# Performance work log

Measured on AMD Instinct MI355X. Metric: run time of the kernel, lower is better.

The kernel has to match this reference:

```python
import jax, jax.numpy as jnp
import numpy as np

B, S, C, L, E, A, H = 4, 4, 4, 512, 64, 32, 8


def _xavier(k, shape, fan_in, fan_out):
    lim = float(np.sqrt(6.0 / (fan_in + fan_out)))
    return jax.random.uniform(k, shape, jnp.float32, -lim, lim)


def setup_inputs() -> dict:
    key = jax.random.key(0)
    ks = jax.random.split(key, 14)
    inp = {
        "query_sequences": jax.random.normal(ks[0], (B, S, L, E), jnp.float32),
        "key_sequences": jax.random.normal(ks[1], (B, S, L, E), jnp.float32),
        "value_sequences": jax.random.normal(ks[2], (B, S, L, E), jnp.float32),
        "query_constants": jax.random.normal(ks[3], (B, C, 1, E), jnp.float32),
        "key_constants": jax.random.normal(ks[4], (B, C, 1, E), jnp.float32),
        "value_constants": jax.random.normal(ks[5], (B, C, 1, E), jnp.float32),
        "qw_seq": _xavier(ks[6], (S, H, E, A), E, A),
        "kw_seq": _xavier(ks[7], (S, H, E, A), E, A),
        "vw_seq": _xavier(ks[8], (S, H, E, A), E, A),
        "qw_con": _xavier(ks[9], (C, H, E, A), E, A),
        "kw_con": _xavier(ks[10], (C, H, E, A), E, A),
        "vw_con": _xavier(ks[11], (C, H, E, A), E, A),
        "head_w_seq": _xavier(ks[12], (S, H * A, E), H * A, E),
        "head_w_con": _xavier(ks[13], (C, H * A, E), H * A, E),
        "mask": 1,
    }
    return inp


def reference(query_sequences, key_sequences, value_sequences,
              query_constants, key_constants, value_constants,
              qw_seq, kw_seq, vw_seq, qw_con, kw_con, vw_con,
              head_w_seq, head_w_con, mask):
    # Per-sequence / per-constant, per-head QKV projections
    q_s = jnp.einsum('bsle,shea->bshla', query_sequences, qw_seq)      # [B,S,H,L,A]
    q_c = jnp.einsum('bcle,chea->bchla', query_constants, qw_con)      # [B,C,H,1,A]
    k_s = jnp.einsum('bsle,shea->bhsla', key_sequences, kw_seq).reshape(B, H, S * L, A)
    k_c = jnp.einsum('bcle,chea->bhcla', key_constants, kw_con).reshape(B, H, C, A)
    v_s = jnp.einsum('bsle,shea->bhsla', value_sequences, vw_seq).reshape(B, H, S * L, A)
    v_c = jnp.einsum('bcle,chea->bhcla', value_constants, vw_con).reshape(B, H, C, A)
    k_all = jnp.concatenate([k_s, k_c], axis=2)                        # [B,H,K,A], K=S*L+C
    v_all = jnp.concatenate([v_s, v_c], axis=2)

    scale = 1.0 / jnp.sqrt(jnp.asarray(A, jnp.float32))
    scores_s = jnp.einsum('bshla,bhka->bshlk', q_s, k_all) * scale     # [B,S,H,L,K]
    if mask:
        # block-causal: within each of the S key blocks mask future timesteps;
        # constant columns (time index -1) are always visible.
        kt = jnp.concatenate([jnp.tile(jnp.arange(L), S), jnp.full((C,), -1)])
        m = kt[None, :] > jnp.arange(L)[:, None]                       # [L,K]
        scores_s = jnp.where(m, -jnp.inf, scores_s)
    p_s = jax.nn.softmax(scores_s, axis=-1)
    out_s = jnp.einsum('bshlk,bhka->bslha', p_s, v_all).reshape(B, S, L, H * A)
    seq_out = jnp.einsum('bslf,sfe->bsle', out_s, head_w_seq)          # [B,S,L,E]

    scores_c = jnp.einsum('bchla,bhka->bchlk', q_c, k_all) * scale     # [B,C,H,1,K]
    p_c = jax.nn.softmax(scores_c, axis=-1)
    out_c = jnp.einsum('bchlk,bhka->bclha', p_c, v_all).reshape(B, C, 1, H * A)
    con_out = jnp.einsum('bclf,cfe->bcle', out_c, head_w_con)          # [B,C,1,E]
    return (seq_out, con_out)
```

## Files before the change

kernel.cpp:

```cpp
#include <hip/hip_runtime.h>
#include <hip/hip_bf16.h>

#define B_ 4
#define S_ 4
#define C_ 4
#define L_ 512
#define E_ 64
#define A_ 32
#define H_ 8
#define HA_ 256
#define KREAL 2052
#define KP 2112
#define NKT 33
#define SCALE 0.17677669529663687f
#define SCALE2 0.25503486321392056f
#define NEGINF (-__builtin_inff())

using bf16  = __bf16;
using bf16x8 = __attribute__((ext_vector_type(8))) __bf16;
using f32x4  = __attribute__((ext_vector_type(4))) float;

#define OFF_QS    0ull
#define OFF_KALL  4194304ull
#define OFF_VT    8519680ull
#define OFF_OUTS  12845056ull
#define OFF_OUTC  17039360ull

__device__ __forceinline__ bool detect_f32_fast(const unsigned int* __restrict__ x0)
{
  unsigned v = x0[threadIdx.x & 63];
  int e = (int)((v >> 7) & 0xFF);
  bool weird = (e == 0xFF || e < 0x60 || e > 0x9F);
  unsigned long long m = __ballot(weird);
  return __builtin_popcountll(m) > 16;
}

__device__ __forceinline__ bf16x8 ld8(const void* p, size_t idx, bool isf32) {
  if (isf32) {
    const float* f = (const float*)p + idx;
    float4 lo = *(const float4*)f;
    float4 hi = *(const float4*)(f + 4);
    bf16x8 v;
    v[0] = (bf16)lo.x; v[1] = (bf16)lo.y; v[2] = (bf16)lo.z; v[3] = (bf16)lo.w;
    v[4] = (bf16)hi.x; v[5] = (bf16)hi.y; v[6] = (bf16)hi.z; v[7] = (bf16)hi.w;
    return v;
  }
  return *(const bf16x8*)((const bf16*)p + idx);
}
__device__ __forceinline__ float ldf(const void* p, size_t idx, bool isf32) {
  return isf32 ? ((const float*)p)[idx] : (float)((const bf16*)p)[idx];
}

__global__ __launch_bounds__(256) void proj_kernel(
    const void* __restrict__ xq, const void* __restrict__ xk, const void* __restrict__ xv,
    const void* __restrict__ kc_in, const void* __restrict__ vc_in,
    const void* __restrict__ wq, const void* __restrict__ wk, const void* __restrict__ wv,
    const void* __restrict__ wkc, const void* __restrict__ wvc,
    bf16* __restrict__ qs, bf16* __restrict__ kall, bf16* __restrict__ vt)
{
  bool isf32 = detect_f32_fast((const unsigned int*)xq);
  int bid = blockIdx.x;
  int tid = threadIdx.x;
  if (bid < 1024) {
    int h = bid & 7, lc8 = (bid >> 3) & 7, s = (bid >> 6) & 3, b = (bid >> 8) & 3;
    __shared__ bf16 wt[3 * 32 * 72];
    __shared__ bf16 v_lds[32 * 72];
    {
      size_t hb = (size_t)(s * H_ + h) * E_ * A_;
      int e = tid >> 2, ac = tid & 3;
      bf16x8 vq = ld8(wq, hb + e * 32 + ac * 8, isf32);
      bf16x8 vk = ld8(wk, hb + e * 32 + ac * 8, isf32);
      bf16x8 vv = ld8(wv, hb + e * 32 + ac * 8, isf32);
#pragma unroll
      for (int j = 0; j < 8; ++j) {
        int a = ac * 8 + j;
        wt[0 * 2304 + a * 72 + e] = vq[j];
        wt[1 * 2304 + a * 72 + e] = vk[j];
        wt[2 * 2304 + a * 72 + e] = vv[j];
      }
    }
    __syncthreads();
    int lane = tid & 63, wave = tid >> 6;
    int quad = lane >> 4, r = lane & 15;
    const size_t xbase = (size_t)(b * S_ + s) * L_ * E_;
    const size_t qsb   = (size_t)((b * S_ + s) * H_ + h) * L_ * A_;
    const size_t kab   = (size_t)(b * H_ + h) * KP * A_;
    const size_t vtb   = (size_t)(b * H_ + h) * A_ * KP;
    int lloc0 = wave * 16;
    int row0 = lc8 * 64 + lloc0;
    size_t rowoff = xbase + (size_t)(row0 + r) * E_ + quad * 8;
    bf16x8 aq0 = ld8(xq, rowoff, isf32);
    bf16x8 aq1 = ld8(xq, rowoff + 32, isf32);
    bf16x8 ak0 = ld8(xk, rowoff, isf32);
    bf16x8 ak1 = ld8(xk, rowoff + 32, isf32);
    bf16x8 av0 = ld8(xv, rowoff, isf32);
    bf16x8 av1 = ld8(xv, rowoff + 32, isf32);
#pragma unroll
    for (int nt = 0; nt < 2; ++nt) {
      bf16x8 bq0 = *(const bf16x8*)&wt[(nt * 16 + r) * 72 + 0 + quad * 8];
      bf16x8 bq1 = *(const bf16x8*)&wt[(nt * 16 + r) * 72 + 32 + quad * 8];
      bf16x8 bk0 = *(const bf16x8*)&wt[2304 + (nt * 16 + r) * 72 + 0 + quad * 8];
      bf16x8 bk1 = *(const bf16x8*)&wt[2304 + (nt * 16 + r) * 72 + 32 + quad * 8];
      bf16x8 bv0 = *(const bf16x8*)&wt[4608 + (nt * 16 + r) * 72 + 0 + quad * 8];
      bf16x8 bv1 = *(const bf16x8*)&wt[4608 + (nt * 16 + r) * 72 + 32 + quad * 8];
      f32x4 accq = {0.f,0.f,0.f,0.f}, acck = {0.f,0.f,0.f,0.f}, accv = {0.f,0.f,0.f,0.f};
      accq = __builtin_amdgcn_mfma_f32_16x16x32_bf16(aq0, bq0, accq, 0,0,0);
      accq = __builtin_amdgcn_mfma_f32_16x16x32_bf16(aq1, bq1, accq, 0,0,0);
      acck = __builtin_amdgcn_mfma_f32_16x16x32_bf16(ak0, bk0, acck, 0,0,0);
      acck = __builtin_amdgcn_mfma_f32_16x16x32_bf16(ak1, bk1, acck, 0,0,0);
      accv = __builtin_amdgcn_mfma_f32_16x16x32_bf16(av0, bv0, accv, 0,0,0);
      accv = __builtin_amdgcn_mfma_f32_16x16x32_bf16(av1, bv1, accv, 0,0,0);
#pragma unroll
      for (int reg = 0; reg < 4; ++reg) {
        int l = row0 + quad * 4 + reg;
        int a = nt * 16 + r;
        qs[qsb + (size_t)l * A_ + a]              = (bf16)(accq[reg] * SCALE2);
        kall[kab + (size_t)(s * L_ + l) * A_ + a] = (bf16)acck[reg];
        v_lds[a * 72 + lloc0 + quad * 4 + reg]    = (bf16)accv[reg];
      }
    }
    __syncthreads();
    {
      int a = tid >> 3, c8 = tid & 7;
      *(bf16x8*)&vt[vtb + (size_t)a * KP + s * L_ + lc8 * 64 + c8 * 8] =
          *(const bf16x8*)&v_lds[a * 72 + c8 * 8];
    }
  } else {
    int cid = bid - 1024;
    int b = cid >> 5, c = (cid >> 3) & 3, h = cid & 7;
    if (tid < 32) {
      int a = tid;
      float kacc = 0.f, vacc = 0.f;
#pragma unroll 8
      for (int e = 0; e < E_; ++e) {
        float xke = ldf(kc_in, (b * C_ + c) * E_ + e, isf32);
        float xve = ldf(vc_in, (b * C_ + c) * E_ + e, isf32);
        float wke = ldf(wkc, ((size_t)(c * H_ + h) * E_ + e) * A_ + a, isf32);
        float wve = ldf(wvc, ((size_t)(c * H_ + h) * E_ + e) * A_ + a, isf32);
        kacc += xke * wke;
        vacc += xve * wve;
      }
      kall[((size_t)(b * H_ + h) * KP + (S_ * L_ + c)) * A_ + a] = (bf16)kacc;
      vt[((size_t)(b * H_ + h) * A_ + a) * KP + (S_ * L_ + c)]   = (bf16)vacc;
    }
    if (c == 0) {
      for (int idx = tid; idx < 60 * 32; idx += 256) {
        int k = KREAL + (idx >> 5), a = idx & 31;
        kall[((size_t)(b * H_ + h) * KP + k) * A_ + a] = (bf16)0.f;
        vt[((size_t)(b * H_ + h) * A_ + a) * KP + k]   = (bf16)0.f;
      }
    }
  }
}

__global__ __launch_bounds__(256) void attn_kernel(
    const bf16* __restrict__ qs, const bf16* __restrict__ kall, const bf16* __restrict__ vt,
    const int* __restrict__ maskp, bf16* __restrict__ outs,
    const void* __restrict__ qc_raw, const void* __restrict__ wqc_raw,
    const unsigned int* __restrict__ x0, float* __restrict__ outc)
{
  __shared__ __attribute__((aligned(16))) bf16 kt_lds[64 * 40];
  __shared__ __attribute__((aligned(16))) bf16 vt_lds[32 * 72];
  __shared__ __attribute__((aligned(16))) bf16 p_lds[4 * 16 * 72];
  int bid = blockIdx.x, tid = threadIdx.x;
  int lane = tid & 63, wave = tid >> 6, quad = lane >> 4, r = lane & 15;
  if (bid < 1024) {
    int h = bid & 7;
    int q0 = (bid >> 3) & 7;
    int s = (bid >> 6) & 3;
    int b = (bid >> 8) & 3;
    int base = (q0 + 2 * (b >> 1)) & 7;
    int qt = (b & 1) ? 7 - base : base;
    bool causal = (*maskp != 0);
    int wrow = qt * 64 + wave * 16;
    int lrow = wrow + r;
    int blockmax = qt * 64 + 63;

    const size_t qsb = (size_t)((b * S_ + s) * H_ + h) * L_ * A_;
    bf16x8 aq = *(const bf16x8*)&qs[qsb + (size_t)(wrow + r) * A_ + quad * 8];

    f32x4 o[2];
    { f32x4 z = {0.f,0.f,0.f,0.f}; o[0] = z; o[1] = z; }
    float l_run = 0.f;

    const size_t kbase = (size_t)(b * H_ + h) * KP * A_;
    const size_t vbase = (size_t)(b * H_ + h) * A_ * KP;
    const int pbase = wave * 16 * 72;

#pragma unroll 1
    for (int kt = 0; kt < NKT; ++kt) {
      int kmod = (kt & 7) * 64;
      if (causal && kt < 32 && kmod > blockmax) continue;
      __syncthreads();
      {
        int krow = tid >> 2, c4 = tid & 3;
        *(bf16x8*)&kt_lds[krow * 40 + c4 * 8] =
            *(const bf16x8*)&kall[kbase + (size_t)(kt * 64 + krow) * A_ + c4 * 8];
        int a8 = tid >> 3, c8 = tid & 7;
        *(bf16x8*)&vt_lds[a8 * 72 + c8 * 8] =
            *(const bf16x8*)&vt[vbase + (size_t)a8 * KP + kt * 64 + c8 * 8];
      }
      __syncthreads();
      if (causal && kt < 32 && kmod >= wrow + 16) continue;
      bool fullv = (kt < 32) && (!causal || kmod + 63 <= wrow);

      f32x4 sf[4];
#pragma unroll
      for (int kg = 0; kg < 4; ++kg) {
        bf16x8 ka = *(const bf16x8*)&kt_lds[(kg * 16 + r) * 40 + quad * 8];
        f32x4 z = {0.f,0.f,0.f,0.f};
        sf[kg] = __builtin_amdgcn_mfma_f32_16x16x32_bf16(ka, aq, z, 0,0,0);
      }
      if (!fullv) {
        int thresh = (kt < 32) ? (lrow - kmod) : 3;
#pragma unroll
        for (int kg = 0; kg < 4; ++kg)
#pragma unroll
          for (int reg = 0; reg < 4; ++reg)
            if (kg * 16 + quad * 4 + reg > thresh) sf[kg][reg] = NEGINF;
      }
      float psum = 0.f;
#pragma unroll
      for (int kg = 0; kg < 4; ++kg) {
        float p0 = exp2f(sf[kg][0]);
        float p1 = exp2f(sf[kg][1]);
        float p2 = exp2f(sf[kg][2]);
        float p3 = exp2f(sf[kg][3]);
        psum += (p0 + p1) + (p2 + p3);
        union { bf16 hh[4]; uint2 u2; } pk;
        pk.hh[0] = (bf16)p0; pk.hh[1] = (bf16)p1; pk.hh[2] = (bf16)p2; pk.hh[3] = (bf16)p3;
        *(uint2*)&p_lds[pbase + r * 72 + kg * 16 + quad * 4] = pk.u2;
      }
      psum += __shfl_xor(psum, 16);
      psum += __shfl_xor(psum, 32);
      l_run += psum;
#pragma unroll
      for (int kc2 = 0; kc2 < 2; ++kc2) {
        bf16x8 ap = *(const bf16x8*)&p_lds[pbase + r * 72 + kc2 * 32 + quad * 8];
#pragma unroll
        for (int nt = 0; nt < 2; ++nt) {
          bf16x8 bv = *(const bf16x8*)&vt_lds[(nt * 16 + r) * 72 + kc2 * 32 + quad * 8];
          o[nt] = __builtin_amdgcn_mfma_f32_16x16x32_bf16(ap, bv, o[nt], 0,0,0);
        }
      }
    }
    const size_t obase = (size_t)(b * S_ + s) * L_ * HA_;
#pragma unroll
    for (int reg = 0; reg < 4; ++reg) {
      float lo = __shfl(l_run, (lane & 48) | (quad * 4 + reg));
      int orow = wrow + quad * 4 + reg;
#pragma unroll
      for (int nt = 0; nt < 2; ++nt) {
        int f = h * A_ + nt * 16 + r;
        outs[obase + (size_t)orow * HA_ + f] = (bf16)(o[nt][reg] / lo);
      }
    }
  } else {
    bool isf32 = detect_f32_fast(x0);
    float* parr  = (float*)p_lds;
    float* qsh   = (float*)kt_lds;
    float* red   = (float*)kt_lds + 64;
    float* opart = (float*)kt_lds + 128;
    int cid = bid - 1024;
    int b = cid >> 5, c = (cid >> 3) & 3, h = cid & 7;
    if (tid < 32) {
      float acc = 0.f;
#pragma unroll 8
      for (int e = 0; e < E_; ++e)
        acc += ldf(qc_raw, (b * C_ + c) * E_ + e, isf32) *
               ldf(wqc_raw, ((size_t)(c * H_ + h) * E_ + e) * A_ + tid, isf32);
      qsh[tid] = acc * SCALE;
    }
    if (tid >= 192 && tid < 192 + (KP - KREAL)) parr[KREAL + tid - 192] = 0.f;
    __syncthreads();
    const size_t kbase = (size_t)(b * H_ + h) * KP * A_;
    float lmax = -1e30f;
#pragma unroll 1
    for (int j = 0; j < 9; ++j) {
      int k = tid + j * 256;
      if (k < KREAL) {
        bf16x8 k0 = *(const bf16x8*)&kall[kbase + (size_t)k * A_ + 0];
        bf16x8 k1 = *(const bf16x8*)&kall[kbase + (size_t)k * A_ + 8];
        bf16x8 k2 = *(const bf16x8*)&kall[kbase + (size_t)k * A_ + 16];
        bf16x8 k3 = *(const bf16x8*)&kall[kbase + (size_t)k * A_ + 24];
        float d = 0.f;
#pragma unroll
        for (int i = 0; i < 8; ++i) {
          d += qsh[i]      * (float)k0[i];
          d += qsh[8 + i]  * (float)k1[i];
          d += qsh[16 + i] * (float)k2[i];
          d += qsh[24 + i] * (float)k3[i];
        }
        parr[k] = d;
        lmax = fmaxf(lmax, d);
      }
    }
#pragma unroll
    for (int dlt = 1; dlt < 64; dlt <<= 1) lmax = fmaxf(lmax, __shfl_xor(lmax, dlt));
    if (lane == 0) red[wave] = lmax;
    __syncthreads();
    float bmax = fmaxf(fmaxf(red[0], red[1]), fmaxf(red[2], red[3]));
    float lsum = 0.f;
#pragma unroll 1
    for (int j = 0; j < 9; ++j) {
      int k = tid + j * 256;
      if (k < KREAL) {
        float p = __expf(parr[k] - bmax);
        parr[k] = p;
        lsum += p;
      }
    }
#pragma unroll
    for (int dlt = 1; dlt < 64; dlt <<= 1) lsum += __shfl_xor(lsum, dlt);
    if (lane == 0) red[4 + wave] = lsum;
    __syncthreads();
    float bsum = (red[4] + red[5]) + (red[6] + red[7]);
    int a = tid >> 3, ch = tid & 7;
    const size_t vbase = (size_t)(b * H_ + h) * A_ * KP + (size_t)a * KP;
    float acc = 0.f;
#pragma unroll 1
    for (int j = 0; j < 33; ++j) {
      int kb = ch * 8 + j * 64;
      bf16x8 vv = *(const bf16x8*)&vt[vbase + kb];
      float4 p0 = *(float4*)&parr[kb];
      float4 p1 = *(float4*)&parr[kb + 4];
      acc += p0.x * (float)vv[0] + p0.y * (float)vv[1] + p0.z * (float)vv[2] + p0.w * (float)vv[3];
      acc += p1.x * (float)vv[4] + p1.y * (float)vv[5] + p1.z * (float)vv[6] + p1.w * (float)vv[7];
    }
    opart[a * 9 + ch] = acc;
    __syncthreads();
    if (tid < 32) {
      float t = 0.f;
#pragma unroll
      for (int i = 0; i < 8; ++i) t += opart[tid * 9 + i];
      outc[(size_t)(b * C_ + c) * HA_ + h * A_ + tid] = t / bsum;
    }
  }
}

__global__ __launch_bounds__(256) void hproj_kernel(
    const bf16* __restrict__ outs, const float* __restrict__ outc,
    const void* __restrict__ hws_raw, const void* __restrict__ hwc_raw,
    const unsigned int* __restrict__ x0, void* __restrict__ out)
{
  __shared__ __attribute__((aligned(16))) bf16 wt[32 * 264];
  bool isf32 = detect_f32_fast(x0);
  int bid = blockIdx.x, tid = threadIdx.x;
  if (bid < 512) {
    int eh = bid & 1, rc = (bid >> 1) & 15, s = (bid >> 5) & 3, b = (bid >> 7) & 3;
    for (int idx = tid; idx < HA_ * 4; idx += 256) {
      int f = idx >> 2, ec = idx & 3;
      bf16x8 v = ld8(hws_raw, (size_t)s * HA_ * E_ + (size_t)f * E_ + eh * 32 + ec * 8, isf32);
#pragma unroll
      for (int j = 0; j < 8; ++j) wt[(ec * 8 + j) * 264 + f] = v[j];
    }
    __syncthreads();
    int lane = tid & 63, wave = tid >> 6, quad = lane >> 4, r = lane & 15;
    int rowh = wave & 1, ntw = wave >> 1;
    int row0 = rc * 32 + rowh * 16;
    const size_t xbase = (size_t)(b * S_ + s) * L_ * HA_;
    bf16x8 af[8];
#pragma unroll
    for (int kc = 0; kc < 8; ++kc)
      af[kc] = *(const bf16x8*)&outs[xbase + (size_t)(row0 + r) * HA_ + kc * 32 + quad * 8];
    f32x4 acc = {0.f,0.f,0.f,0.f};
#pragma unroll
    for (int kc = 0; kc < 8; ++kc) {
      bf16x8 bfr = *(const bf16x8*)&wt[(ntw * 16 + r) * 264 + kc * 32 + quad * 8];
      acc = __builtin_amdgcn_mfma_f32_16x16x32_bf16(af[kc], bfr, acc, 0,0,0);
    }
#pragma unroll
    for (int reg = 0; reg < 4; ++reg) {
      int row = row0 + quad * 4 + reg;
      int e = eh * 32 + ntw * 16 + r;
      size_t oidx = ((size_t)(b * S_ + s) * L_ + row) * E_ + e;
      if (isf32) ((float*)out)[oidx] = acc[reg];
      else       ((bf16*)out)[oidx]  = (bf16)acc[reg];
    }
  } else {
    float* opart = (float*)wt;
    int i2 = bid - 512;
    int b = i2 >> 2, c = i2 & 3;
    int fc = tid >> 6, e = tid & 63;
    const float* oc = outc + (size_t)(b * C_ + c) * HA_;
    float acc = 0.f;
#pragma unroll 4
    for (int fo = 0; fo < 64; ++fo) {
      int f = fc * 64 + fo;
      acc += oc[f] * ldf(hwc_raw, ((size_t)c * HA_ + f) * E_ + e, isf32);
    }
    opart[fc * 68 + e] = acc;
    __syncthreads();
    if (tid < 64) {
      float t = (opart[0 * 68 + tid] + opart[1 * 68 + tid]) +
                (opart[2 * 68 + tid] + opart[3 * 68 + tid]);
      size_t oidx = (size_t)B_ * S_ * L_ * E_ + (size_t)(b * C_ + c) * E_ + tid;
      if (isf32) ((float*)out)[oidx] = t;
      else       ((bf16*)out)[oidx]  = (bf16)t;
    }
  }
}

extern "C" void kernel_launch(void* const* d_in, const int* in_sizes, int n_in,
                              void* d_out, int out_size, void* d_ws, size_t ws_size,
                              hipStream_t stream) {
  char* ws = (char*)d_ws;
  bf16* qs    = (bf16*)(ws + OFF_QS);
  bf16* kall  = (bf16*)(ws + OFF_KALL);
  bf16* vt    = (bf16*)(ws + OFF_VT);
  bf16* outs  = (bf16*)(ws + OFF_OUTS);
  float* outc = (float*)(ws + OFF_OUTC);
  const int* maskp = (const int*)d_in[14];
  const unsigned int* x0 = (const unsigned int*)d_in[0];

  proj_kernel<<<1152, 256, 0, stream>>>(d_in[0], d_in[1], d_in[2], d_in[4], d_in[5],
                                        d_in[6], d_in[7], d_in[8], d_in[10], d_in[11],
                                        qs, kall, vt);
  attn_kernel<<<1152, 256, 0, stream>>>(qs, kall, vt, maskp, outs,
                                        d_in[3], d_in[9], x0, outc);
  hproj_kernel<<<528, 256, 0, stream>>>(outs, outc, d_in[12], d_in[13], x0, d_out);
}
```

Before: 161.9 us.

## Process two key tiles per barrier pair over a compact active-tile schedule

The attention loop now enumerates only the key tiles that are active under the block-causal mask, plus the constants tile, instead of iterating all 33 and skipping. It loads two K/V tiles into registers before the barrier and stages both into enlarged LDS buffers, so each pair of __syncthreads covers two tiles. The aim is to halve barrier count, issue global loads earlier, and remove idle skipped iterations. In exchange, LDS use per block is higher, and the constants path now reuses different shared arrays for its scratch space.

```diff
diff --git a/kernel.cpp b/kernel.cpp
--- a/kernel.cpp
+++ b/kernel.cpp
@@ -159,8 +159,8 @@
     const void* __restrict__ qc_raw, const void* __restrict__ wqc_raw,
     const unsigned int* __restrict__ x0, float* __restrict__ outc)
 {
-  __shared__ __attribute__((aligned(16))) bf16 kt_lds[64 * 40];
-  __shared__ __attribute__((aligned(16))) bf16 vt_lds[32 * 72];
+  __shared__ __attribute__((aligned(16))) bf16 kt_lds[128 * 40];
+  __shared__ __attribute__((aligned(16))) bf16 vt_lds[32 * 136];
   __shared__ __attribute__((aligned(16))) bf16 p_lds[4 * 16 * 72];
   int bid = blockIdx.x, tid = threadIdx.x;
   int lane = tid & 63, wave = tid >> 6, quad = lane >> 4, r = lane & 15;
@@ -174,7 +174,6 @@
     bool causal = (*maskp != 0);
     int wrow = qt * 64 + wave * 16;
     int lrow = wrow + r;
-    int blockmax = qt * 64 + 63;
 
     const size_t qsb = (size_t)((b * S_ + s) * H_ + h) * L_ * A_;
     bf16x8 aq = *(const bf16x8*)&qs[qsb + (size_t)(wrow + r) * A_ + quad * 8];
@@ -186,28 +185,17 @@
     const size_t kbase = (size_t)(b * H_ + h) * KP * A_;
     const size_t vbase = (size_t)(b * H_ + h) * A_ * KP;
     const int pbase = wave * 16 * 72;
-
-#pragma unroll 1
-    for (int kt = 0; kt < NKT; ++kt) {
+    int rowg = tid >> 2, c4 = tid & 3;
+    int a8 = tid >> 3, c8 = tid & 7;
+
+    auto compute_tile = [&](int kt, int half) {
       int kmod = (kt & 7) * 64;
-      if (causal && kt < 32 && kmod > blockmax) continue;
-      __syncthreads();
-      {
-        int krow = tid >> 2, c4 = tid & 3;
-        *(bf16x8*)&kt_lds[krow * 40 + c4 * 8] =
-            *(const bf16x8*)&kall[kbase + (size_t)(kt * 64 + krow) * A_ + c4 * 8];
-        int a8 = tid >> 3, c8 = tid & 7;
-        *(bf16x8*)&vt_lds[a8 * 72 + c8 * 8] =
-            *(const bf16x8*)&vt[vbase + (size_t)a8 * KP + kt * 64 + c8 * 8];
-      }
-      __syncthreads();
-      if (causal && kt < 32 && kmod >= wrow + 16) continue;
+      if (causal && kt < 32 && kmod >= wrow + 16) return;
       bool fullv = (kt < 32) && (!causal || kmod + 63 <= wrow);
-
       f32x4 sf[4];
 #pragma unroll
       for (int kg = 0; kg < 4; ++kg) {
-        bf16x8 ka = *(const bf16x8*)&kt_lds[(kg * 16 + r) * 40 + quad * 8];
+        bf16x8 ka = *(const bf16x8*)&kt_lds[(half * 64 + kg * 16 + r) * 40 + quad * 8];
         f32x4 z = {0.f,0.f,0.f,0.f};
         sf[kg] = __builtin_amdgcn_mfma_f32_16x16x32_bf16(ka, aq, z, 0,0,0);
       }
@@ -239,10 +227,40 @@
         bf16x8 ap = *(const bf16x8*)&p_lds[pbase + r * 72 + kc2 * 32 + quad * 8];
 #pragma unroll
         for (int nt = 0; nt < 2; ++nt) {
-          bf16x8 bv = *(const bf16x8*)&vt_lds[(nt * 16 + r) * 72 + kc2 * 32 + quad * 8];
+          bf16x8 bv = *(const bf16x8*)&vt_lds[(nt * 16 + r) * 136 + half * 64 + kc2 * 32 + quad * 8];
           o[nt] = __builtin_amdgcn_mfma_f32_16x16x32_bf16(ap, bv, o[nt], 0,0,0);
         }
       }
+    };
+
+    int qtc = causal ? qt : 7;
+    int nact = 4 * (qtc + 1) + 1;
+    int g = 0, mn = 0, ktcur = 0;
+#pragma unroll 1
+    for (int i = 0; i < nact; i += 2) {
+      int ktA = ktcur;
+      bool haveB = (i + 1 < nact);
+      int ktB = ktA;
+      if (haveB) {
+        mn++; if (mn > qtc) { mn = 0; g++; }
+        ktB = (g >= 4) ? 32 : g * 8 + mn;
+      }
+      if (i + 2 < nact) {
+        mn++; if (mn > qtc) { mn = 0; g++; }
+        ktcur = (g >= 4) ? 32 : g * 8 + mn;
+      }
+      bf16x8 kAr = *(const bf16x8*)&kall[kbase + (size_t)(ktA * 64 + rowg) * A_ + c4 * 8];
+      bf16x8 kBr = *(const bf16x8*)&kall[kbase + (size_t)(ktB * 64 + rowg) * A_ + c4 * 8];
+      bf16x8 vAr = *(const bf16x8*)&vt[vbase + (size_t)a8 * KP + ktA * 64 + c8 * 8];
+      bf16x8 vBr = *(const bf16x8*)&vt[vbase + (size_t)a8 * KP + ktB * 64 + c8 * 8];
+      __syncthreads();
+      *(bf16x8*)&kt_lds[rowg * 40 + c4 * 8]        = kAr;
+      *(bf16x8*)&kt_lds[(64 + rowg) * 40 + c4 * 8] = kBr;
+      *(bf16x8*)&vt_lds[a8 * 136 + c8 * 8]         = vAr;
+      *(bf16x8*)&vt_lds[a8 * 136 + 64 + c8 * 8]    = vBr;
+      __syncthreads();
+      compute_tile(ktA, 0);
+      if (haveB) compute_tile(ktB, 1);
     }
     const size_t obase = (size_t)(b * S_ + s) * L_ * HA_;
 #pragma unroll
@@ -257,10 +275,10 @@
     }
   } else {
     bool isf32 = detect_f32_fast(x0);
-    float* parr  = (float*)p_lds;
-    float* qsh   = (float*)kt_lds;
-    float* red   = (float*)kt_lds + 64;
-    float* opart = (float*)kt_lds + 128;
+    float* parr  = (float*)kt_lds;
+    float* qsh   = (float*)vt_lds;
+    float* red   = (float*)vt_lds + 64;
+    float* opart = (float*)vt_lds + 128;
     int cid = bid - 1024;
     int b = cid >> 5, c = (cid >> 3) & 3, h = cid & 7;
     if (tid < 32) {
```

Measured after the change: 160.9 us. Within noise of the previous version (-0.6%).
